# Kernel optimization log

Measured on AMD Instinct MI355X. Metric: run time of the kernel, lower is better.

The kernel has to match this reference:

```python
import jax, jax.numpy as jnp
import numpy as np

C_SPARSITY = 3.0  # repo default
N_BLOCKS_1 = 128   # layer_inputs // granularity
IN_PER_BLK_1 = 64  # granularity
LAYER_OUTPUTS = 8192

def setup_inputs() -> dict:
    key = jax.random.key(0)
    k_x, k_c1, k_c2 = jax.random.split(key, 3)
    x = jax.random.normal(k_x, (4096, 8192), dtype=jnp.float32)
    # c_sub_layer_1: [n_blocks_1, inputs_per_block_1, outputs_per_block_1]
    c1 = jax.random.normal(k_c1, (128, 64, 64), dtype=jnp.float32)
    # c_sub_layer_2: [n_blocks_2, inputs_per_block_2, outputs_per_block_2]
    c2 = jax.random.normal(k_c2, (64, 128, 128), dtype=jnp.float32)
    return {"x": x, "c1": c1, "c2": c2}

def reference(x, c1, c2):
    # Softmax-gated connectivity over the input axis of each block (dim=1)
    conn_1 = jax.nn.softmax(c1 * C_SPARSITY, axis=1)  # [n, i, m]
    conn_2 = jax.nn.softmax(c2 * C_SPARSITY, axis=1)  # [m, n, o]
    b = x.shape[0]
    x_r = x.reshape(b, N_BLOCKS_1, IN_PER_BLK_1)  # [b, n, i]
    # Two-stage block-diagonal interconnect (Monarch-like)
    t = jnp.einsum('bni,nim->bnm', x_r, conn_1)   # [b, n, m]
    out = jnp.einsum('bnm,mno->bmo', t, conn_2)   # [b, m, o]
    return out.reshape(b, LAYER_OUTPUTS)
```

## Files before the change

### kernel.cpp

```cpp
#include <hip/hip_runtime.h>

#define BATCH     4096
#define N1        128
#define I1        64
#define MMID      64
#define OOUT      128
#define LDX       8192
#define CSP       3.0f

typedef _Float16 half8  __attribute__((ext_vector_type(8)));
typedef float    float4_ __attribute__((ext_vector_type(4)));
typedef unsigned int uint4_ __attribute__((ext_vector_type(4)));

__global__ __launch_bounds__(256) void prep_kernel(
    const float* __restrict__ c1, const float* __restrict__ c2,
    _Float16* __restrict__ conn1T, _Float16* __restrict__ conn2T) {
  int gid = blockIdx.x * 256 + threadIdx.x;
  if (gid < N1 * MMID) {
    const float* p = c1 + (size_t)(gid >> 6) * (I1 * MMID) + (gid & 63);
    float mx = -1e30f;
    for (int i = 0; i < I1; ++i) mx = fmaxf(mx, p[i * MMID]);
    mx *= CSP;
    float s = 0.f;
    for (int i = 0; i < I1; ++i) s += __expf(p[i * MMID] * CSP - mx);
    float inv = 1.0f / s;
    _Float16* dst = conn1T + (size_t)gid * I1;
    for (int i = 0; i < I1; ++i)
      dst[i] = (_Float16)(__expf(p[i * MMID] * CSP - mx) * inv);
  } else {
    int g = gid - N1 * MMID;
    if (g < MMID * OOUT) {
      const float* p = c2 + (size_t)(g >> 7) * (N1 * OOUT) + (g & 127);
      float mx = -1e30f;
      for (int i = 0; i < N1; ++i) mx = fmaxf(mx, p[i * OOUT]);
      mx *= CSP;
      float s = 0.f;
      for (int i = 0; i < N1; ++i) s += __expf(p[i * OOUT] * CSP - mx);
      float inv = 1.0f / s;
      _Float16* dst = conn2T + (size_t)g * N1;
      for (int i = 0; i < N1; ++i)
        dst[i] = (_Float16)(__expf(p[i * OOUT] * CSP - mx) * inv);
    }
  }
}

#define S1_NC      16
#define S1_MSTRIDE 18
#define S1_BSTRIDE (64 * S1_MSTRIDE + 4)

__global__ __launch_bounds__(256) void stage1_kernel(
    const float* __restrict__ x, const _Float16* __restrict__ conn1T,
    _Float16* __restrict__ t2) {
  __shared__ _Float16 lbuf[16 * S1_BSTRIDE];

  const int b0   = blockIdx.x * 16;
  const int c    = blockIdx.y;
  const int n0   = c * S1_NC;
  const int tid  = threadIdx.x;
  const int lane = tid & 63;
  const int wave = tid >> 6;
  const int row  = lane & 15;
  const int quad = lane >> 4;
  const int kk   = quad * 8;

  const float* xrow = x + (size_t)(b0 + row) * LDX;

#pragma unroll 2
  for (int j = 0; j < 4; ++j) {
    const int nn = wave * 4 + j;
    const int n  = n0 + nn;
    const float* ap = xrow + n * I1 + kk;
    float4_ a0lo = *(const float4_*)(ap);
    float4_ a0hi = *(const float4_*)(ap + 4);
    float4_ a1lo = *(const float4_*)(ap + 32);
    float4_ a1hi = *(const float4_*)(ap + 36);
    half8 a0, a1;
#pragma unroll
    for (int u = 0; u < 4; ++u) {
      a0[u]     = (_Float16)a0lo[u];
      a0[u + 4] = (_Float16)a0hi[u];
      a1[u]     = (_Float16)a1lo[u];
      a1[u + 4] = (_Float16)a1hi[u];
    }
    const _Float16* bn = conn1T + (size_t)n * (MMID * I1);
    half8 bf0[4], bf1[4];
#pragma unroll
    for (int mt = 0; mt < 4; ++mt) {
      const _Float16* bp = bn + (mt * 16 + row) * I1 + kk;
      bf0[mt] = *(const half8*)(bp);
      bf1[mt] = *(const half8*)(bp + 32);
    }
#pragma unroll
    for (int mt = 0; mt < 4; ++mt) {
      float4_ acc = {0.f, 0.f, 0.f, 0.f};
      acc = __builtin_amdgcn_mfma_f32_16x16x32_f16(a0, bf0[mt], acc, 0, 0, 0);
      acc = __builtin_amdgcn_mfma_f32_16x16x32_f16(a1, bf1[mt], acc, 0, 0, 0);
#pragma unroll
      for (int r = 0; r < 4; ++r) {
        lbuf[(quad * 4 + r) * S1_BSTRIDE + (mt * 16 + row) * S1_MSTRIDE + nn] =
            (_Float16)acc[r];
      }
    }
  }
  __syncthreads();

#pragma unroll
  for (int it = 0; it < 4; ++it) {
    int p  = tid + it * 256;
    int bl = p >> 6;
    int mm = p & 63;
    const unsigned int* src =
        (const unsigned int*)(lbuf + bl * S1_BSTRIDE + mm * S1_MSTRIDE);
    uint4_ v0 = {src[0], src[1], src[2], src[3]};
    uint4_ v1 = {src[4], src[5], src[6], src[7]};
    _Float16* dst =
        t2 + (((size_t)c * BATCH + b0 + bl) * MMID + mm) * S1_NC;
    *(uint4_*)(dst)     = v0;
    *(uint4_*)(dst + 8) = v1;
  }
}

__global__ __launch_bounds__(256) void stage2_kernel(
    const _Float16* __restrict__ t2, const _Float16* __restrict__ conn2T,
    float* __restrict__ out) {
  const int m    = blockIdx.x;
  const int b0   = blockIdx.y * 64;
  const int tid  = threadIdx.x;
  const int lane = tid & 63;
  const int wave = tid >> 6;
  const int row  = lane & 15;
  const int quad = lane >> 4;

  const int b = b0 + wave * 16 + row;
  half8 a[4];
#pragma unroll
  for (int ks = 0; ks < 4; ++ks) {
    const int cc  = ks * 2 + (quad >> 1);
    const int off = (quad & 1) * 8;
    a[ks] = *(const half8*)(
        t2 + (((size_t)cc * BATCH + b) * MMID + m) * S1_NC + off);
  }
  const _Float16* bbase = conn2T + (size_t)m * OOUT * N1;
  half8 bf[4][8];
#pragma unroll
  for (int ks = 0; ks < 4; ++ks)
#pragma unroll
    for (int ot = 0; ot < 8; ++ot)
      bf[ks][ot] =
          *(const half8*)(bbase + (size_t)(ot * 16 + row) * N1 + ks * 32 + quad * 8);

  float4_ acc[8];
#pragma unroll
  for (int ot = 0; ot < 8; ++ot) acc[ot] = (float4_){0.f, 0.f, 0.f, 0.f};
#pragma unroll
  for (int ks = 0; ks < 4; ++ks)
#pragma unroll
    for (int ot = 0; ot < 8; ++ot)
      acc[ot] = __builtin_amdgcn_mfma_f32_16x16x32_f16(a[ks], bf[ks][ot], acc[ot], 0, 0, 0);

#pragma unroll
  for (int ot = 0; ot < 8; ++ot) {
#pragma unroll
    for (int r = 0; r < 4; ++r) {
      const int bb = b0 + wave * 16 + quad * 4 + r;
      const int o  = ot * 16 + row;
      out[(size_t)bb * LDX + m * OOUT + o] = acc[ot][r];
    }
  }
}

extern "C" void kernel_launch(void* const* d_in, const int* in_sizes, int n_in,
                              void* d_out, int out_size, void* d_ws, size_t ws_size,
                              hipStream_t stream) {
  (void)in_sizes; (void)n_in; (void)out_size; (void)ws_size;
  const float* x  = (const float*)d_in[0];
  const float* c1 = (const float*)d_in[1];
  const float* c2 = (const float*)d_in[2];
  float* out = (float*)d_out;

  _Float16* conn1T = (_Float16*)d_ws;
  _Float16* conn2T = conn1T + (size_t)N1 * MMID * I1;
  _Float16* t2     = conn2T + (size_t)MMID * OOUT * N1;

  prep_kernel<<<64, 256, 0, stream>>>(c1, c2, conn1T, conn2T);
  stage1_kernel<<<dim3(BATCH / 16, N1 / S1_NC), 256, 0, stream>>>(x, conn1T, t2);
  stage2_kernel<<<dim3(MMID, BATCH / 64), 256, 0, stream>>>(t2, conn2T, out);
}
```

Baseline: 357.6 us.

## Fuse both Monarch stages into one kernel with LDS-resident intermediate

Replaces the separate stage1 and stage2 kernels with a single fused kernel. Each block computes a 16-row batch tile for a quarter of the mid dimension (16 m values), stores the fp16 intermediate in a swizzled LDS buffer, and then runs the second block-diagonal matmul directly from LDS. This removes the global write and read of the t2 intermediate and one kernel launch. In exchange, each block now re-reads all of its x rows (so x is read four times across the m-quarters, with block ordering chosen to help L2 reuse) and streams conn2 weights from global memory inside the MFMA loop.

New measurement: 370.7 us. 3.7% more time.

```diff
diff --git a/kernel.cpp b/kernel.cpp
--- a/kernel.cpp
+++ b/kernel.cpp
@@ -9,8 +9,8 @@
 #define CSP       3.0f
 
 typedef _Float16 half8  __attribute__((ext_vector_type(8)));
+typedef _Float16 half4_ __attribute__((ext_vector_type(4)));
 typedef float    float4_ __attribute__((ext_vector_type(4)));
-typedef unsigned int uint4_ __attribute__((ext_vector_type(4)));
 
 __global__ __launch_bounds__(256) void prep_kernel(
     const float* __restrict__ c1, const float* __restrict__ c2,
@@ -44,18 +44,16 @@
   }
 }
 
-#define S1_NC      16
-#define S1_MSTRIDE 18
-#define S1_BSTRIDE (64 * S1_MSTRIDE + 4)
+__global__ __launch_bounds__(256, 2) void fused_kernel(
+    const float* __restrict__ x, const _Float16* __restrict__ conn1T,
+    const _Float16* __restrict__ conn2T, float* __restrict__ out) {
+  __shared__ _Float16 tl[16 * 16 * 128];
 
-__global__ __launch_bounds__(256) void stage1_kernel(
-    const float* __restrict__ x, const _Float16* __restrict__ conn1T,
-    _Float16* __restrict__ t2) {
-  __shared__ _Float16 lbuf[16 * S1_BSTRIDE];
-
-  const int b0   = blockIdx.x * 16;
-  const int c    = blockIdx.y;
-  const int n0   = c * S1_NC;
+  const int bid  = blockIdx.x;
+  const int bt   = ((bid >> 5) << 3) | (bid & 7);
+  const int q    = (bid >> 3) & 3;
+  const int b0   = bt * 16;
+  const int m0   = q * 16;
   const int tid  = threadIdx.x;
   const int lane = tid & 63;
   const int wave = tid >> 6;
@@ -64,107 +62,79 @@
   const int kk   = quad * 8;
 
   const float* xrow = x + (size_t)(b0 + row) * LDX;
+  const _Float16* w1m = conn1T + (size_t)(m0 + row) * I1 + kk;
 
 #pragma unroll 2
-  for (int j = 0; j < 4; ++j) {
-    const int nn = wave * 4 + j;
-    const int n  = n0 + nn;
-    const float* ap = xrow + n * I1 + kk;
-    float4_ a0lo = *(const float4_*)(ap);
-    float4_ a0hi = *(const float4_*)(ap + 4);
-    float4_ a1lo = *(const float4_*)(ap + 32);
-    float4_ a1hi = *(const float4_*)(ap + 36);
-    half8 a0, a1;
+  for (int g = 0; g < 8; ++g) {
+    const int n0 = wave * 32 + g * 4;
+    float4_ acc4[4];
 #pragma unroll
-    for (int u = 0; u < 4; ++u) {
-      a0[u]     = (_Float16)a0lo[u];
-      a0[u + 4] = (_Float16)a0hi[u];
-      a1[u]     = (_Float16)a1lo[u];
-      a1[u + 4] = (_Float16)a1hi[u];
-    }
-    const _Float16* bn = conn1T + (size_t)n * (MMID * I1);
-    half8 bf0[4], bf1[4];
+    for (int nn = 0; nn < 4; ++nn) {
+      const int n = n0 + nn;
+      const float* ap = xrow + n * I1 + kk;
+      float4_ a0lo = *(const float4_*)(ap);
+      float4_ a0hi = *(const float4_*)(ap + 4);
+      float4_ a1lo = *(const float4_*)(ap + 32);
+      float4_ a1hi = *(const float4_*)(ap + 36);
+      half8 a0, a1;
 #pragma unroll
-    for (int mt = 0; mt < 4; ++mt) {
-      const _Float16* bp = bn + (mt * 16 + row) * I1 + kk;
-      bf0[mt] = *(const half8*)(bp);
-      bf1[mt] = *(const half8*)(bp + 32);
+      for (int u = 0; u < 4; ++u) {
+        a0[u]     = (_Float16)a0lo[u];
+        a0[u + 4] = (_Float16)a0hi[u];
+        a1[u]     = (_Float16)a1lo[u];
+        a1[u + 4] = (_Float16)a1hi[u];
+      }
+      const _Float16* bp = w1m + (size_t)n * (MMID * I1);
+      half8 bf0 = *(const half8*)(bp);
+      half8 bf1 = *(const half8*)(bp + 32);
+      float4_ acc = {0.f, 0.f, 0.f, 0.f};
+      acc = __builtin_amdgcn_mfma_f32_16x16x32_f16(a0, bf0, acc, 0, 0, 0);
+      acc = __builtin_amdgcn_mfma_f32_16x16x32_f16(a1, bf1, acc, 0, 0, 0);
+      acc4[nn] = acc;
     }
 #pragma unroll
-    for (int mt = 0; mt < 4; ++mt) {
-      float4_ acc = {0.f, 0.f, 0.f, 0.f};
-      acc = __builtin_amdgcn_mfma_f32_16x16x32_f16(a0, bf0[mt], acc, 0, 0, 0);
-      acc = __builtin_amdgcn_mfma_f32_16x16x32_f16(a1, bf1[mt], acc, 0, 0, 0);
-#pragma unroll
-      for (int r = 0; r < 4; ++r) {
-        lbuf[(quad * 4 + r) * S1_BSTRIDE + (mt * 16 + row) * S1_MSTRIDE + nn] =
-            (_Float16)acc[r];
-      }
+    for (int r = 0; r < 4; ++r) {
+      const int b    = quad * 4 + r;
+      const int swz  = ((b + row) & 7) << 4;
+      const int byte = (b * 16 + row) * 256 + ((n0 * 2) ^ swz);
+      half4_ v = { (_Float16)acc4[0][r], (_Float16)acc4[1][r],
+                   (_Float16)acc4[2][r], (_Float16)acc4[3][r] };
+      *(half4_*)((char*)tl + byte) = v;
     }
   }
   __syncthreads();
 
 #pragma unroll
-  for (int it = 0; it < 4; ++it) {
-    int p  = tid + it * 256;
-    int bl = p >> 6;
-    int mm = p & 63;
-    const unsigned int* src =
-        (const unsigned int*)(lbuf + bl * S1_BSTRIDE + mm * S1_MSTRIDE);
-    uint4_ v0 = {src[0], src[1], src[2], src[3]};
-    uint4_ v1 = {src[4], src[5], src[6], src[7]};
-    _Float16* dst =
-        t2 + (((size_t)c * BATCH + b0 + bl) * MMID + mm) * S1_NC;
-    *(uint4_*)(dst)     = v0;
-    *(uint4_*)(dst + 8) = v1;
-  }
-}
-
-__global__ __launch_bounds__(256) void stage2_kernel(
-    const _Float16* __restrict__ t2, const _Float16* __restrict__ conn2T,
-    float* __restrict__ out) {
-  const int m    = blockIdx.x;
-  const int b0   = blockIdx.y * 64;
-  const int tid  = threadIdx.x;
-  const int lane = tid & 63;
-  const int wave = tid >> 6;
-  const int row  = lane & 15;
-  const int quad = lane >> 4;
-
-  const int b = b0 + wave * 16 + row;
-  half8 a[4];
+  for (int mi = 0; mi < 4; ++mi) {
+    const int ml = wave * 4 + mi;
+    const int mg = m0 + ml;
+    half8 af[4];
 #pragma unroll
-  for (int ks = 0; ks < 4; ++ks) {
-    const int cc  = ks * 2 + (quad >> 1);
-    const int off = (quad & 1) * 8;
-    a[ks] = *(const half8*)(
-        t2 + (((size_t)cc * BATCH + b) * MMID + m) * S1_NC + off);
-  }
-  const _Float16* bbase = conn2T + (size_t)m * OOUT * N1;
-  half8 bf[4][8];
+    for (int ks = 0; ks < 4; ++ks) {
+      const int swz  = ((row + ml) & 7) << 4;
+      const int byte = (row * 16 + ml) * 256 + ((ks * 64 + quad * 16) ^ swz);
+      af[ks] = *(const half8*)((const char*)tl + byte);
+    }
+    const _Float16* bbase =
+        conn2T + (size_t)mg * (OOUT * N1) + (size_t)row * N1 + kk;
+    float4_ acc[8];
 #pragma unroll
-  for (int ks = 0; ks < 4; ++ks)
+    for (int ot = 0; ot < 8; ++ot) acc[ot] = (float4_){0.f, 0.f, 0.f, 0.f};
 #pragma unroll
-    for (int ot = 0; ot < 8; ++ot)
-      bf[ks][ot] =
-          *(const half8*)(bbase + (size_t)(ot * 16 + row) * N1 + ks * 32 + quad * 8);
-
-  float4_ acc[8];
+    for (int ks = 0; ks < 4; ++ks) {
 #pragma unroll
-  for (int ot = 0; ot < 8; ++ot) acc[ot] = (float4_){0.f, 0.f, 0.f, 0.f};
+      for (int ot = 0; ot < 8; ++ot) {
+        half8 bf = *(const half8*)(bbase + (size_t)(ot * 16) * N1 + ks * 32);
+        acc[ot] = __builtin_amdgcn_mfma_f32_16x16x32_f16(af[ks], bf, acc[ot], 0, 0, 0);
+      }
+    }
+    float* obase = out + (size_t)b0 * LDX + (size_t)mg * OOUT + row;
 #pragma unroll
-  for (int ks = 0; ks < 4; ++ks)
+    for (int ot = 0; ot < 8; ++ot) {
 #pragma unroll
-    for (int ot = 0; ot < 8; ++ot)
-      acc[ot] = __builtin_amdgcn_mfma_f32_16x16x32_f16(a[ks], bf[ks][ot], acc[ot], 0, 0, 0);
-
-#pragma unroll
-  for (int ot = 0; ot < 8; ++ot) {
-#pragma unroll
-    for (int r = 0; r < 4; ++r) {
-      const int bb = b0 + wave * 16 + quad * 4 + r;
-      const int o  = ot * 16 + row;
-      out[(size_t)bb * LDX + m * OOUT + o] = acc[ot][r];
+      for (int r = 0; r < 4; ++r) {
+        obase[(size_t)(quad * 4 + r) * LDX + ot * 16] = acc[ot][r];
+      }
     }
   }
 }
@@ -180,9 +150,7 @@
 
   _Float16* conn1T = (_Float16*)d_ws;
   _Float16* conn2T = conn1T + (size_t)N1 * MMID * I1;
-  _Float16* t2     = conn2T + (size_t)MMID * OOUT * N1;
 
   prep_kernel<<<64, 256, 0, stream>>>(c1, c2, conn1T, conn2T);
-  stage1_kernel<<<dim3(BATCH / 16, N1 / S1_NC), 256, 0, stream>>>(x, conn1T, t2);
-  stage2_kernel<<<dim3(MMID, BATCH / 64), 256, 0, stream>>>(t2, conn2T, out);
+  fused_kernel<<<dim3(BATCH / 16 * 4), 256, 0, stream>>>(x, conn1T, conn2T, out);
 }
```
